# Kernel optimization log

Measured on AMD Instinct MI355X. Metric: run time of the kernel, lower is better.

## Reference

```python
import jax, jax.numpy as jnp
import numpy as np

N_SIGMA = 2
FG_W = 1.0
W_INST, W_VAR, W_SEED = 1.0, 10.0, 1.0
N_IDS = 15  # instance ids 1..15 (0 = background)


def _xym(H, W, dtype):
    # torch buffer: xm varies along width, ym along height, linspace over 512 then sliced
    xm = jnp.broadcast_to(jnp.linspace(0.0, 1.0, 512)[:W][None, :], (H, W))
    ym = jnp.broadcast_to(jnp.linspace(0.0, 1.0, 512)[:H][:, None], (H, W))
    return jnp.stack([xm, ym], 0).astype(dtype)  # [2,H,W]


def _lovasz_hinge_flat(logits, gt):
    # canonical Lovasz hinge over a flat image; gt in {0,1} float
    signs = 2.0 * gt - 1.0
    errors = 1.0 - logits * signs
    order = jnp.argsort(-errors)
    errors_sorted = errors[order]
    gt_sorted = gt[order]
    gts = gt_sorted.sum()
    inter = gts - jnp.cumsum(gt_sorted)
    union = gts + jnp.cumsum(1.0 - gt_sorted)
    jacc = 1.0 - inter / union
    grad = jnp.concatenate([jacc[:1], jacc[1:] - jacc[:-1]])
    return jnp.dot(jax.nn.relu(errors_sorted), jax.lax.stop_gradient(grad))


def _loss(prediction, instances, labels):
    B, C, H, W = prediction.shape
    xym = _xym(H, W, prediction.dtype)
    spatial_emb = jnp.tanh(prediction[:, 0:2]) + xym           # [B,2,H,W]
    sigma = prediction[:, 2:2 + N_SIGMA]                       # [B,2,H,W]
    seed = jax.nn.sigmoid(prediction[:, 2 + N_SIGMA])          # [B,H,W]

    ids = jnp.arange(1, N_IDS + 1)
    maskf = (instances[:, None] == ids[None, :, None, None]).astype(prediction.dtype)  # [B,N,H,W]
    counts = maskf.sum((-2, -1))                               # [B,N]
    valid = counts > 0
    safe = jnp.maximum(counts, 1.0)

    centers = jnp.einsum('bchw,bnhw->bnc', spatial_emb, maskf) / safe[..., None]  # [B,N,2]
    s_mean = jnp.einsum('bchw,bnhw->bnc', sigma, maskf) / safe[..., None]         # [B,N,2]
    s_sg = jax.lax.stop_gradient(s_mean)

    # sum over mask of (sigma - s_sg)^2, expanded to avoid a [B,N,2,H,W] tensor
    e2 = jnp.einsum('bchw,bnhw->bnc', sigma * sigma, maskf)
    var_sum = e2 - 2.0 * s_sg * (s_mean * safe[..., None]) + s_sg * s_sg * counts[..., None]
    var_i = var_sum.sum(-1) / (N_SIGMA * safe)                 # torch.mean over [n_sigma, M]

    s_exp = jnp.exp(10.0 * s_mean)                             # [B,N,2] (grad flows, as in torch)
    dist_arg = jnp.zeros((B, N_IDS, H, W), prediction.dtype)
    for c in range(N_SIGMA):  # tiny fixed loop over 2 coordinate channels
        d = spatial_emb[:, c][:, None] - centers[:, :, c][..., None, None]
        dist_arg = dist_arg + s_exp[:, :, c][..., None, None] * d * d
    dist = jnp.exp(-dist_arg)                                  # [B,N,H,W]

    logits = (dist * 2.0 - 1.0).reshape(B * N_IDS, H * W)
    labs = maskf.reshape(B * N_IDS, H * W)
    inst_i = jax.vmap(_lovasz_hinge_flat)(logits, labs).reshape(B, N_IDS)

    seed_i = FG_W * jnp.einsum('bnhw,bnhw->bn', maskf,
                               (seed[:, None] - jax.lax.stop_gradient(dist)) ** 2)

    bg = (labels == 0).astype(prediction.dtype)
    seed_bg = jnp.einsum('bhw,bhw->b', bg, seed * seed)        # (seed - 0)^2 on background

    vf = valid.astype(prediction.dtype)
    obj = jnp.maximum(vf.sum(1), 1.0)
    inst_b = (vf * inst_i).sum(1) / obj
    var_b = (vf * var_i).sum(1) / obj
    seed_b = (seed_bg + (vf * seed_i).sum(1)) / (H * W)
    return jnp.mean(W_INST * inst_b + W_VAR * var_b + W_SEED * seed_b)


def setup_inputs() -> dict:
    key = jax.random.key(0)
    k1, k2, k3 = jax.random.split(key, 3)
    prediction = jax.random.normal(k1, (16, 5, 512, 512), dtype=jnp.float32)
    instances = jax.random.randint(k2, (16, 512, 512), 0, 16, dtype=jnp.int64)
    labels = jax.random.randint(k3, (16, 512, 512), 0, 2, dtype=jnp.int64)
    return {"prediction": prediction, "instances": instances, "labels": labels}


def reference(prediction, instances, labels):
    return _loss(prediction, instances, labels)
```

## Files before the change

### kernel.cpp

```cpp
#include <hip/hip_runtime.h>
#include <hip/hip_fp16.h>
#include <cmath>

#define BATCH 16
#define NID   15
#define NSEG  240
#define HW    262144
#define HEADB 65536
#define NSPL  8
#define NCHK  4
#define PREBLK 512
#define PSTRIDE 112

#define KFINEBASE 30208
#define KOVF 119
#define KTOT 2424

__device__ __forceinline__ int keyof(float d) {
  unsigned b = __float_as_uint(d);
  return (b >= 0x3B800000u) ? (int)((b >> 15) - KFINEBASE + KOVF) : (int)(b >> 23);
}
__device__ __forceinline__ void boundsof(int k, float* lo, float* hi) {
  if (k >= KOVF) {
    unsigned u = (unsigned)(k - KOVF + KFINEBASE) << 15;
    *lo = __uint_as_float(u);
    *hi = __uint_as_float(u + 32768u);
  } else {
    *lo = __uint_as_float((unsigned)k << 23);
    *hi = __uint_as_float((unsigned)(k + 1) << 23);
  }
}

__device__ __forceinline__ float fast_tanh(float x) {
  float e = __expf(2.0f * x);
  return 1.0f - 2.0f / (e + 1.0f);
}
__device__ __forceinline__ float fast_sigmoid(float x) {
  return 1.0f / (1.0f + __expf(-x));
}

struct Params { float cx, cy, e0, e1, var, valid, cnt; };
__device__ __forceinline__ Params calc_params(const float* __restrict__ st) {
  Params p;
  float cnt = st[0];
  float safe = fmaxf(cnt, 1.0f);
  p.cx = st[1] / safe;
  p.cy = st[2] / safe;
  float m0 = st[3] / safe, m1 = st[4] / safe;
  float v0 = st[5] - 2.0f * m0 * (m0 * safe) + m0 * m0 * cnt;
  float v1 = st[6] - 2.0f * m1 * (m1 * safe) + m1 * m1 * cnt;
  p.var = (v0 + v1) / (2.0f * safe);
  p.e0 = expf(10.0f * m0);
  p.e1 = expf(10.0f * m1);
  p.valid = (cnt > 0.f) ? 1.f : 0.f;
  p.cnt = cnt;
  return p;
}

__global__ void __launch_bounds__(256, 2)
pre_kernel(const float* __restrict__ pred, const int* __restrict__ inst,
           const int* __restrict__ lab, float* __restrict__ blockpart,
           unsigned* __restrict__ exyh, unsigned* __restrict__ tb8,
           unsigned* __restrict__ sd8) {
  __shared__ float ws[4][NID * 7 + 1];
  int tid = threadIdx.x;
  int w = tid >> 6, lane = tid & 63;
  int gid = blockIdx.x;
  int b = gid >> 5, c = gid & 31;
  const float* pb = pred + (size_t)b * 5 * HW;
  const int4* ip = (const int4*)(inst + (size_t)b * HW);
  const int4* lp = (const int4*)(lab + (size_t)b * HW);
  size_t bq = (size_t)b * (HW / 4);
  float acc[NID][7];
#pragma unroll
  for (int id = 0; id < NID; ++id)
#pragma unroll
    for (int s = 0; s < 7; ++s) acc[id][s] = 0.f;
  float bgacc = 0.f;
  for (int it = 0; it < 8; ++it) {
    int g = c * 2048 + it * 256 + tid;
    float4 v0 = ((const float4*)pb)[g];
    float4 v1 = ((const float4*)(pb + HW))[g];
    float4 v2 = ((const float4*)(pb + 2 * HW))[g];
    float4 v3 = ((const float4*)(pb + 3 * HW))[g];
    float4 v4 = ((const float4*)(pb + 4 * HW))[g];
    int4 t4 = ip[g];
    int4 l4 = lp[g];
    float p0a[4] = {v0.x, v0.y, v0.z, v0.w};
    float p1a[4] = {v1.x, v1.y, v1.z, v1.w};
    float p2a[4] = {v2.x, v2.y, v2.z, v2.w};
    float p3a[4] = {v3.x, v3.y, v3.z, v3.w};
    float p4a[4] = {v4.x, v4.y, v4.z, v4.w};
    int ta[4] = {t4.x, t4.y, t4.z, t4.w};
    int la[4] = {l4.x, l4.y, l4.z, l4.w};
    unsigned eo[4], tpack = 0, spack = 0;
    int px0 = g * 4;
#pragma unroll
    for (int k = 0; k < 4; ++k) {
      int px = px0 + k;
      float xm = (float)(px & 511) * (1.0f / 511.0f);
      float ym = (float)(px >> 9) * (1.0f / 511.0f);
      float ex = fast_tanh(p0a[k]) + xm;
      float ey = fast_tanh(p1a[k]) + ym;
      float sd = fast_sigmoid(p4a[k]);
      __half2 h = __floats2half2_rn(ex, ey);
      eo[k] = *reinterpret_cast<unsigned*>(&h);
      int t = ta[k];
      tpack |= ((unsigned)(t & 255)) << (8 * k);
      unsigned sq = (unsigned)(sd * 255.0f + 0.5f);
      spack |= (sq & 255u) << (8 * k);
      float p2 = p2a[k], p3 = p3a[k];
      float q2 = p2 * p2, q3 = p3 * p3;
#pragma unroll
      for (int id = 0; id < NID; ++id) {
        float pr = (t == id + 1) ? 1.0f : 0.0f;
        acc[id][0] += pr;
        acc[id][1] += pr * ex;
        acc[id][2] += pr * ey;
        acc[id][3] += pr * p2;
        acc[id][4] += pr * p3;
        acc[id][5] += pr * q2;
        acc[id][6] += pr * q3;
      }
      if (la[k] == 0) bgacc += sd * sd;
    }
    ((uint4*)exyh)[bq + g] = make_uint4(eo[0], eo[1], eo[2], eo[3]);
    tb8[bq + g] = tpack;
    sd8[bq + g] = spack;
  }
#pragma unroll
  for (int id = 0; id < NID; ++id)
#pragma unroll
    for (int s = 0; s < 7; ++s) {
      float v = acc[id][s];
      for (int off = 32; off > 0; off >>= 1) v += __shfl_down(v, off, 64);
      if (lane == 0) ws[w][id * 7 + s] = v;
    }
  for (int off = 32; off > 0; off >>= 1) bgacc += __shfl_down(bgacc, off, 64);
  if (lane == 0) ws[w][NID * 7] = bgacc;
  __syncthreads();
  float* bp = blockpart + (size_t)gid * PSTRIDE;
  for (int i = tid; i < NID * 7 + 1; i += 256)
    bp[i] = ws[0][i] + ws[1][i] + ws[2][i] + ws[3][i];
}

__global__ void reduce_kernel(const float* __restrict__ blockpart, float* __restrict__ stats,
                              float* __restrict__ seedbg) {
  int s = blockIdx.x;
  int b = blockIdx.y;
  int tid = threadIdx.x;
  float v = (tid < 32) ? blockpart[(size_t)(b * 32 + tid) * PSTRIDE + s] : 0.f;
  for (int off = 32; off > 0; off >>= 1) v += __shfl_down(v, off, 64);
  if (tid == 0) {
    if (s < NID * 7) {
      int id = s / 7, st = s % 7;
      stats[(b * NID + id) * 8 + st] = v;
    } else {
      seedbg[b] = v;
    }
  }
}

__global__ void __launch_bounds__(512)
hist_kernel(const unsigned* __restrict__ exyh, const unsigned* __restrict__ tb8,
            const unsigned* __restrict__ sd8, const float* __restrict__ stats,
            unsigned* __restrict__ partPN, float* __restrict__ seedi) {
  int split = blockIdx.x;
  int chunk = blockIdx.y;
  int b = blockIdx.z;
  int seg0 = chunk * 4;
  __shared__ unsigned lhist[4 * KTOT];
  __shared__ float prm[4][5];
  int tid = threadIdx.x;
  if (tid < 4) {
    int gs = seg0 + tid;
    if (gs < NID) {
      Params pp = calc_params(stats + (size_t)(b * NID + gs) * 8);
      prm[tid][0] = pp.cx; prm[tid][1] = pp.cy; prm[tid][2] = pp.e0; prm[tid][3] = pp.e1;
      prm[tid][4] = pp.valid;
    } else {
      prm[tid][4] = 0.f;
    }
  }
  for (int k = tid; k < 4 * KTOT; k += 512) lhist[k] = 0u;
  __syncthreads();
  float cxr[4], cyr[4], e0r[4], e1r[4];
  bool vr[4];
#pragma unroll
  for (int n = 0; n < 4; ++n) {
    cxr[n] = prm[n][0]; cyr[n] = prm[n][1]; e0r[n] = prm[n][2]; e1r[n] = prm[n][3];
    vr[n] = (prm[n][4] != 0.f);
  }
  const uint4* ev = (const uint4*)exyh + (size_t)b * (HW / 4);
  const unsigned* tv = tb8 + (size_t)b * (HW / 4);
  const unsigned* sv = sd8 + (size_t)b * (HW / 4);
  int lane = tid & 63;
  int wid = tid >> 6;
  int swl = (lane * 21) & 63;
  float sacc[4] = {0.f, 0.f, 0.f, 0.f};
  int g = split * 8192 + wid * 64 + swl;
  uint4 ee = ev[g];
  unsigned tp = tv[g];
  unsigned sp = sv[g];
  for (int it = 0; it < 16; ++it) {
    uint4 ne; unsigned ntp, nsp;
    int ng = g + 512;
    if (it < 15) { ne = ev[ng]; ntp = tv[ng]; nsp = sv[ng]; }
    unsigned ew[4] = {ee.x, ee.y, ee.z, ee.w};
#pragma unroll
    for (int k = 0; k < 4; ++k) {
      unsigned u = ew[k];
      __half2 h = *reinterpret_cast<__half2*>(&u);
      float2 e = __half22float2(h);
      int t = (int)((tp >> (8 * k)) & 255u);
#pragma unroll
      for (int n = 0; n < 4; ++n) {
        if (!vr[n]) continue;
        float dx = e.x - cxr[n];
        float dy = e.y - cyr[n];
        float d = __expf(-(e0r[n] * dx * dx + e1r[n] * dy * dy));
        int key = keyof(d);
        bool pos = (t == seg0 + n + 1);
        atomicAdd(&lhist[n * KTOT + key], pos ? 65536u : 1u);
        if (pos) {
          float sd = (float)((sp >> (8 * k)) & 255u) * (1.0f / 255.0f);
          float df = sd - d;
          sacc[n] += df * df;
        }
      }
    }
    if (it < 15) { ee = ne; tp = ntp; sp = nsp; g = ng; }
  }
#pragma unroll
  for (int n = 0; n < 4; ++n) {
    float v = sacc[n];
    for (int off = 32; off > 0; off >>= 1) v += __shfl_down(v, off, 64);
    if (lane == 0 && v != 0.f) atomicAdd(&seedi[b * NID + seg0 + n], v);
  }
  __syncthreads();
#pragma unroll
  for (int n = 0; n < 4; ++n) {
    int gs = seg0 + n;
    if (gs >= NID) break;
    size_t base = ((size_t)(b * NID + gs) * NSPL + split) * KTOT;
    for (int k = tid; k < KTOT; k += 512) partPN[base + k] = lhist[n * KTOT + k];
  }
}

__global__ void __launch_bounds__(1024)
lovasz_kernel(const unsigned* __restrict__ partPN, const float* __restrict__ stats,
              float* __restrict__ instAcc) {
  __shared__ int histP[KTOT];
  __shared__ int histN[KTOT];
  __shared__ int PreP[KTOT + 1];
  __shared__ int PreN[KTOT + 1];
  __shared__ int scr[1024];
  __shared__ float prm[2];
  int seg = blockIdx.x;
  int tid = threadIdx.x;
  if (tid == 0) {
    Params pp = calc_params(stats + (size_t)seg * 8);
    prm[0] = pp.valid;
    prm[1] = pp.cnt;
  }
  __syncthreads();
  if (prm[0] == 0.f) {
    if (tid == 0) instAcc[seg] = 0.f;
    return;
  }
  int P = (int)prm[1];
  int Nn = HW - P;
  for (int k = tid; k < KTOT; k += 1024) {
    int sp = 0, sn = 0;
#pragma unroll
    for (int s = 0; s < NSPL; ++s) {
      unsigned v = partPN[((size_t)seg * NSPL + s) * KTOT + k];
      sp += (int)(v >> 16);
      sn += (int)(v & 0xFFFFu);
    }
    histP[k] = sp;
    histN[k] = sn;
  }
  __syncthreads();
  {
    int base = tid * 3;
    int a0 = (base < KTOT) ? histP[base] : 0;
    int a1 = (base + 1 < KTOT) ? histP[base + 1] : 0;
    int a2 = (base + 2 < KTOT) ? histP[base + 2] : 0;
    scr[tid] = a0 + a1 + a2;
    __syncthreads();
    for (int off = 1; off < 1024; off <<= 1) {
      int v = scr[tid];
      int u = (tid >= off) ? scr[tid - off] : 0;
      __syncthreads();
      scr[tid] = v + u;
      __syncthreads();
    }
    int excl = (tid > 0) ? scr[tid - 1] : 0;
    if (base < KTOT) PreP[base] = excl;
    if (base + 1 < KTOT) PreP[base + 1] = excl + a0;
    if (base + 2 < KTOT) PreP[base + 2] = excl + a0 + a1;
    if (tid == 0) PreP[KTOT] = scr[1023];
    __syncthreads();
    a0 = (base < KTOT) ? histN[base] : 0;
    a1 = (base + 1 < KTOT) ? histN[base + 1] : 0;
    a2 = (base + 2 < KTOT) ? histN[base + 2] : 0;
    scr[tid] = a0 + a1 + a2;
    __syncthreads();
    for (int off = 1; off < 1024; off <<= 1) {
      int v = scr[tid];
      int u = (tid >= off) ? scr[tid - off] : 0;
      __syncthreads();
      scr[tid] = v + u;
      __syncthreads();
    }
    excl = (tid > 0) ? scr[tid - 1] : 0;
    if (base < KTOT) PreN[base] = excl;
    if (base + 1 < KTOT) PreN[base + 1] = excl + a0;
    if (base + 2 < KTOT) PreN[base + 2] = excl + a0 + a1;
    if (tid == 0) PreN[KTOT] = scr[1023];
    __syncthreads();
  }
  float acc = 0.f;
  for (int k = tid; k < KTOT; k += 1024) {
    int hp = histP[k], hn = histN[k];
    if ((hp | hn) == 0) continue;
    float lo, hi;
    boundsof(k, &lo, &hi);
    float m = 0.5f * (lo + hi);
    m = fminf(m, __uint_as_float(0x3F7FFFFFu));
    float tv = 1.0f - m;
    int j = keyof(tv);
    float jlo, jhi;
    boundsof(j, &jlo, &jhi);
    float den = jhi - jlo;
    float fr = (den > 0.f) ? (tv - jlo) / den : 0.5f;
    fr = fminf(fmaxf(fr, 0.f), 1.f);
    if (hp) {
      float q = (float)(Nn - PreN[j + 1]) + (1.0f - fr) * (float)histN[j];
      float a = 2.0f - 2.0f * m;
      acc += (float)hp * a / ((float)P + q);
    }
    if (hn) {
      float p = (float)PreP[j] + fr * (float)histP[j];
      int R = Nn - PreN[k + 1];
      float u0 = 1.0f / (float)(P + R);
      float u1 = 1.0f / (float)(P + R + hn);
      acc += (2.0f * m) * ((float)P - p) * (u0 - u1);
    }
  }
  float* scrf = (float*)scr;
  scrf[tid] = acc;
  __syncthreads();
  for (int s = 512; s > 0; s >>= 1) {
    if (tid < s) scrf[tid] += scrf[tid + s];
    __syncthreads();
  }
  if (tid == 0) instAcc[seg] = scrf[0];
}

__global__ void final_kernel(const float* __restrict__ stats, const float* __restrict__ instAcc,
                             const float* __restrict__ seediAcc, const float* __restrict__ seedbg,
                             float* __restrict__ out) {
  int b = threadIdx.x;
  __shared__ float red[64];
  float lb = 0.f;
  if (b < BATCH) {
    float sv = 0.f, si = 0.f, svar = 0.f, ssd = 0.f;
    for (int n = 0; n < NID; ++n) {
      Params pp = calc_params(stats + (size_t)(b * NID + n) * 8);
      float vf = pp.valid;
      sv += vf;
      si += vf * instAcc[b * NID + n];
      svar += vf * pp.var;
      ssd += vf * seediAcc[b * NID + n];
    }
    float obj = fmaxf(sv, 1.0f);
    lb = si / obj + 10.0f * (svar / obj) + (seedbg[b] + ssd) / (float)HW;
  }
  red[threadIdx.x] = lb;
  __syncthreads();
  for (int s = 32; s > 0; s >>= 1) {
    if (threadIdx.x < s) red[threadIdx.x] += red[threadIdx.x + s];
    __syncthreads();
  }
  if (threadIdx.x == 0) out[0] = red[0] / (float)BATCH;
}

extern "C" void kernel_launch(void* const* d_in, const int* in_sizes, int n_in,
                              void* d_out, int out_size, void* d_ws, size_t ws_size,
                              hipStream_t stream) {
  const float* pred = (const float*)d_in[0];
  const int* inst = (const int*)d_in[1];
  const int* lab = (const int*)d_in[2];
  float* out = (float*)d_out;

  float* wsf = (float*)d_ws;
  float* seediAcc = wsf;
  float* stats = wsf + 240;
  float* instAcc = wsf + 2160;
  float* seedbg = wsf + 2400;
  char* p = (char*)d_ws + HEADB;
  unsigned* exyh = (unsigned*)p;            p += (size_t)BATCH * HW * 4;
  unsigned* tb8 = (unsigned*)p;             p += (size_t)BATCH * HW;
  unsigned* sd8 = (unsigned*)p;             p += (size_t)BATCH * HW;
  unsigned* partPN = (unsigned*)p;          p += (size_t)NSEG * NSPL * KTOT * 4;
  float* blockpart = (float*)p;

  hipMemsetAsync(seediAcc, 0, 240 * sizeof(float), stream);
  pre_kernel<<<PREBLK, 256, 0, stream>>>(pred, inst, lab, blockpart, exyh, tb8, sd8);
  reduce_kernel<<<dim3(NID * 7 + 1, BATCH), 64, 0, stream>>>(blockpart, stats, seedbg);
  hist_kernel<<<dim3(NSPL, NCHK, BATCH), 512, 0, stream>>>(exyh, tb8, sd8, stats, partPN, seediAcc);
  lovasz_kernel<<<NSEG, 1024, 0, stream>>>(partPN, stats, instAcc);
  final_kernel<<<1, 64, 0, stream>>>(stats, instAcc, seediAcc, seedbg, out);
}
```

Measured before the change: 254.0 us.

## Replace per-thread instance accumulators with shared-memory atomics and more blocks

The pre-pass kernel no longer keeps a 15x7 register accumulator per thread with a masked update for every id. Each pixel instead atomically adds its seven statistics into a per-wave shared-memory slot indexed by its instance id, with background pixels going to a dummy slot 0. The grid grows from 32 to 128 blocks per image with a higher occupancy hint, and the reduce kernel sums the larger number of partials. This removes about 105 FMAs per pixel and heavy register pressure, but adds LDS atomic contention, since the 64 lanes of a wave spread over only 16 ids.

Result: slower. 343.2 us (+35.1%).

```diff
diff --git a/kernel.cpp b/kernel.cpp
--- a/kernel.cpp
+++ b/kernel.cpp
@@ -9,7 +9,7 @@
 #define HEADB 65536
 #define NSPL  8
 #define NCHK  4
-#define PREBLK 512
+#define PREBLK 2048
 #define PSTRIDE 112
 
 #define KFINEBASE 30208
@@ -57,28 +57,26 @@
   return p;
 }
 
-__global__ void __launch_bounds__(256, 2)
+__global__ void __launch_bounds__(256, 4)
 pre_kernel(const float* __restrict__ pred, const int* __restrict__ inst,
            const int* __restrict__ lab, float* __restrict__ blockpart,
            unsigned* __restrict__ exyh, unsigned* __restrict__ tb8,
            unsigned* __restrict__ sd8) {
-  __shared__ float ws[4][NID * 7 + 1];
+  __shared__ float ws[4][16 * 7];
+  __shared__ float bgw[4];
   int tid = threadIdx.x;
   int w = tid >> 6, lane = tid & 63;
   int gid = blockIdx.x;
-  int b = gid >> 5, c = gid & 31;
+  int b = gid >> 7, c = gid & 127;
   const float* pb = pred + (size_t)b * 5 * HW;
   const int4* ip = (const int4*)(inst + (size_t)b * HW);
   const int4* lp = (const int4*)(lab + (size_t)b * HW);
   size_t bq = (size_t)b * (HW / 4);
-  float acc[NID][7];
-#pragma unroll
-  for (int id = 0; id < NID; ++id)
-#pragma unroll
-    for (int s = 0; s < 7; ++s) acc[id][s] = 0.f;
+  for (int i = tid; i < 4 * 112; i += 256) ((float*)ws)[i] = 0.f;
+  __syncthreads();
   float bgacc = 0.f;
-  for (int it = 0; it < 8; ++it) {
-    int g = c * 2048 + it * 256 + tid;
+  for (int it = 0; it < 2; ++it) {
+    int g = c * 512 + it * 256 + tid;
     float4 v0 = ((const float4*)pb)[g];
     float4 v1 = ((const float4*)(pb + HW))[g];
     float4 v2 = ((const float4*)(pb + 2 * HW))[g];
@@ -105,43 +103,35 @@
       float sd = fast_sigmoid(p4a[k]);
       __half2 h = __floats2half2_rn(ex, ey);
       eo[k] = *reinterpret_cast<unsigned*>(&h);
-      int t = ta[k];
-      tpack |= ((unsigned)(t & 255)) << (8 * k);
+      int t = ta[k] & 15;
+      tpack |= ((unsigned)(ta[k] & 255)) << (8 * k);
       unsigned sq = (unsigned)(sd * 255.0f + 0.5f);
       spack |= (sq & 255u) << (8 * k);
       float p2 = p2a[k], p3 = p3a[k];
-      float q2 = p2 * p2, q3 = p3 * p3;
-#pragma unroll
-      for (int id = 0; id < NID; ++id) {
-        float pr = (t == id + 1) ? 1.0f : 0.0f;
-        acc[id][0] += pr;
-        acc[id][1] += pr * ex;
-        acc[id][2] += pr * ey;
-        acc[id][3] += pr * p2;
-        acc[id][4] += pr * p3;
-        acc[id][5] += pr * q2;
-        acc[id][6] += pr * q3;
-      }
+      float* dst = &ws[w][t * 7];
+      atomicAdd(dst + 0, 1.0f);
+      atomicAdd(dst + 1, ex);
+      atomicAdd(dst + 2, ey);
+      atomicAdd(dst + 3, p2);
+      atomicAdd(dst + 4, p3);
+      atomicAdd(dst + 5, p2 * p2);
+      atomicAdd(dst + 6, p3 * p3);
       if (la[k] == 0) bgacc += sd * sd;
     }
     ((uint4*)exyh)[bq + g] = make_uint4(eo[0], eo[1], eo[2], eo[3]);
     tb8[bq + g] = tpack;
     sd8[bq + g] = spack;
   }
-#pragma unroll
-  for (int id = 0; id < NID; ++id)
-#pragma unroll
-    for (int s = 0; s < 7; ++s) {
-      float v = acc[id][s];
-      for (int off = 32; off > 0; off >>= 1) v += __shfl_down(v, off, 64);
-      if (lane == 0) ws[w][id * 7 + s] = v;
-    }
   for (int off = 32; off > 0; off >>= 1) bgacc += __shfl_down(bgacc, off, 64);
-  if (lane == 0) ws[w][NID * 7] = bgacc;
+  if (lane == 0) bgw[w] = bgacc;
   __syncthreads();
   float* bp = blockpart + (size_t)gid * PSTRIDE;
-  for (int i = tid; i < NID * 7 + 1; i += 256)
-    bp[i] = ws[0][i] + ws[1][i] + ws[2][i] + ws[3][i];
+  if (tid < NID * 7) {
+    int t = tid / 7 + 1, s = tid - (t - 1) * 7;
+    bp[tid] = ws[0][t * 7 + s] + ws[1][t * 7 + s] + ws[2][t * 7 + s] + ws[3][t * 7 + s];
+  } else if (tid == NID * 7) {
+    bp[NID * 7] = bgw[0] + bgw[1] + bgw[2] + bgw[3];
+  }
 }
 
 __global__ void reduce_kernel(const float* __restrict__ blockpart, float* __restrict__ stats,
@@ -149,7 +139,9 @@
   int s = blockIdx.x;
   int b = blockIdx.y;
   int tid = threadIdx.x;
-  float v = (tid < 32) ? blockpart[(size_t)(b * 32 + tid) * PSTRIDE + s] : 0.f;
+  float v = 0.f;
+  for (int i = tid; i < 128; i += 64)
+    v += blockpart[(size_t)(b * 128 + i) * PSTRIDE + s];
   for (int off = 32; off > 0; off >>= 1) v += __shfl_down(v, off, 64);
   if (tid == 0) {
     if (s < NID * 7) {
```
